# Performance work log

Measured on AMD Instinct MI355X. Metric: run time of the kernel, lower is better.

Reference implementation:

```python
import jax, jax.numpy as jnp
import numpy as np

# FTDEA(e_hidden=300, r_hidden=100, t_hidden=100)
N_NODES = 50000
N_EDGES = 250000
N_EDGES_ALL = 500000
N_REL = 300
EH, RH, TH = 300, 100, 100


def _seg_softmax(logits, seg, num):
    # torch_geometric.utils.softmax: segment-wise stable softmax
    m = jax.ops.segment_max(logits, seg, num_segments=num)
    e = jnp.exp(logits - m[seg])
    s = jax.ops.segment_sum(e, seg, num_segments=num)
    return e / s[seg]


def _gcn(x, j, i, n):
    deg = jax.ops.segment_sum(jnp.ones(i.shape[0], x.dtype), i, num_segments=n)
    dinv = jnp.where(deg > 0, 1.0 / jnp.sqrt(jnp.maximum(deg, 1.0)), 0.0)
    norm = dinv[j] * dinv[i]
    return jax.nn.relu(jax.ops.segment_sum(norm[:, None] * x[j], i, num_segments=n))


def setup_inputs():
    key = jax.random.key(0)
    ks = jax.random.split(key, 32)
    f32 = jnp.float32

    def w(k, shape):
        return jax.random.normal(k, shape, f32) / np.float32(np.sqrt(shape[0]))

    inp = {
        "x": jax.random.normal(ks[0], (N_NODES, EH), f32),
        "edge_index": jax.random.randint(ks[1], (2, N_EDGES), 0, N_NODES),
        "rel": jax.random.randint(ks[2], (N_EDGES,), 0, N_REL),
        "edge_index_all": jax.random.randint(ks[3], (2, N_EDGES_ALL), 0, N_NODES),
        "rel_size": jnp.arange(N_EDGES),
        "hw1_w": w(ks[4], (EH, EH)), "hw1_b": jnp.zeros((EH,), f32),
        "hw2_w": w(ks[5], (EH, EH)), "hw2_b": jnp.zeros((EH,), f32),
        "tc1_w": w(ks[6], (EH, TH)), "tc1_b": jnp.zeros((TH,), f32),
        "sr1_w": w(ks[7], (2 * TH, RH)), "sr1_b": jnp.zeros((RH,), f32),
        "a1_w": w(ks[8], (RH,)), "a5_w": w(ks[9], (RH,)),
        "wr_w": w(ks[10], (RH + 2 * TH, EH)), "wr_b": jnp.zeros((EH,), f32),
        "wr1_w": w(ks[11], (RH + 2 * TH, EH)), "wr1_b": jnp.zeros((EH,), f32),
        "wr2_w": w(ks[12], (RH + 2 * TH, EH)), "wr2_b": jnp.zeros((EH,), f32),
        "ah_w": w(ks[13], (EH,)), "ah1_w": w(ks[14], (EH,)), "at_w": w(ks[15], (EH,)),
        "ar1_w": w(ks[16], (EH,)), "ar2_w": w(ks[17], (EH,)), "ar3_w": w(ks[18], (EH,)),
        "ai_w": w(ks[19], (EH,)), "aj_w": w(ks[20], (EH,)),
        "fc_w": w(ks[21], (2 * EH,)), "fc_b": jnp.zeros((1,), f32),
    }
    return inp


def _forward(x, hw1_w, hw1_b, hw2_w, hw2_b, tc1_w, tc1_b, sr1_w, sr1_b, a1_w, a5_w,
             wr_w, wr_b, wr1_w, wr1_b, wr2_w, wr2_b, ah_w, ah1_w, at_w,
             ar1_w, ar2_w, ar3_w, ai_w, aj_w, fc_w, fc_b,
             edge_index, rel, edge_index_all, rel_size):
    N = x.shape[0]
    E = rel.shape[0]
    h, t = edge_index[0], edge_index[1]
    j, i = edge_index_all[0], edge_index_all[1]
    lrelu = jax.nn.leaky_relu  # slope 0.01 == F.leaky_relu default

    def highway(x1, x2, wg, bg):
        gate = jax.nn.sigmoid(x1 @ wg + bg)
        return gate * x2 + (1.0 - gate) * x1

    x = highway(x, _gcn(x, j, i, N), hw1_w, hw1_b)
    x = highway(x, _gcn(x, j, i, N), hw2_w, hw2_b)

    # --- GATt_to_R. NB: FTDEA overwrites gat_e_to_r output with zeros, so
    # x_res1 input is all-zeros and GAT_E_to_R is mathematically dead code.
    # Also r_in_t1 aliases r_in_t in the torch code, so the in-place per-relation
    # mean loop rewrites BOTH -> r_in_t1 = per-relation mean features.
    s = x @ tc1_w + tc1_b                                    # [N, t]
    cnt = jnp.maximum(jax.ops.segment_sum(jnp.ones(E, x.dtype), rel, num_segments=N_REL), 1.0)[:, None]
    mh = jax.ops.segment_sum(s[h], rel, num_segments=N_REL) / cnt
    mt = jax.ops.segment_sum(s[t], rel, num_segments=N_REL) / cnt
    r_in_t1 = jnp.concatenate([mh, mt], axis=1)[rel]         # [E, 2t]
    x_res2 = r_in_t1 @ sr1_w + sr1_b                         # [E, r]
    x_res1 = jnp.zeros((E, RH), x.dtype)                     # zeroed GAT_E_to_R output
    e1 = x_res2 @ a1_w + x_res1 @ a5_w                       # [E]
    alpha = _seg_softmax(lrelu(e1), rel, N_REL)
    x_type = jax.ops.segment_sum(alpha[:, None] * x_res2[rel_size], rel, num_segments=N_REL)  # spmm
    r_f = jnp.concatenate([x_res1 + x_type[rel], r_in_t1], axis=1)   # [E, r+2t]

    # --- GATr_to_e: three attention rounds (head, tail, head) ---
    def r2e(x_e, wr, br, a_node, a_rel, idx):
        e_r = r_f @ wr + br                                  # [E, e]
        logits = x_e[idx] @ a_node + e_r @ a_rel             # [E]
        a = _seg_softmax(lrelu(logits), idx, N)
        agg = jax.nn.relu(jax.ops.segment_sum(a[:, None] * e_r[rel_size], idx, num_segments=N))
        return x_e + agg

    x = r2e(x, wr_w, wr_b, ah_w, ar1_w, h)
    x = r2e(x, wr1_w, wr1_b, at_w, ar2_w, t)
    x = r2e(x, wr2_w, wr2_b, ah1_w, ar3_w, h)

    # --- GAT_act over edge_index_all ---
    logits = (x @ ai_w)[i] + (x @ aj_w)[j]
    a = _seg_softmax(lrelu(logits), i, N)
    g = jax.nn.relu(jax.ops.segment_sum(a[:, None] * x[j], i, num_segments=N))

    return jnp.concatenate([x, g], axis=1) @ fc_w + fc_b[0]  # [N]


def reference(x, edge_index, rel, edge_index_all, rel_size, hw1_w, hw1_b, hw2_w, hw2_b,
              tc1_w, tc1_b, sr1_w, sr1_b, a1_w, a5_w, wr_w, wr_b, wr1_w, wr1_b,
              wr2_w, wr2_b, ah_w, ah1_w, at_w, ar1_w, ar2_w, ar3_w, ai_w, aj_w, fc_w, fc_b):
    return _forward(x, hw1_w, hw1_b, hw2_w, hw2_b, tc1_w, tc1_b, sr1_w, sr1_b, a1_w, a5_w,
                    wr_w, wr_b, wr1_w, wr1_b, wr2_w, wr2_b, ah_w, ah1_w, at_w,
                    ar1_w, ar2_w, ar3_w, ai_w, aj_w, fc_w, fc_b,
                    edge_index, rel, edge_index_all, rel_size)
```

## Files before the change

### kernel.cpp

```cpp
#include <hip/hip_runtime.h>
#include <hip/hip_bf16.h>

typedef __hip_bfloat16 bf16;
typedef __attribute__((ext_vector_type(8))) short bf16x8_t;
typedef __attribute__((ext_vector_type(8))) unsigned short u16x8;
typedef __attribute__((ext_vector_type(4))) float f32x4_t;

__device__ __forceinline__ float b2f(bf16 v){ return __bfloat162float(v); }
__device__ __forceinline__ bf16 f2b(float v){ return __float2bfloat16(v); }
__device__ __forceinline__ short tobits(float v){ bf16 b = f2b(v); return *(short*)&b; }
__device__ __forceinline__ float us2f(ushort u){ return __uint_as_float(((unsigned)u)<<16); }
__device__ __forceinline__ ushort f2us(float v){ bf16 b = f2b(v); return *(ushort*)&b; }

#define NN 50000
#define NN128 50048
#define NE 250000
#define NEA 500000
#define NR 300
#define EHD 300
#define THD 100
#define RHD 100
#define XP 320
#define ERP 320
#define RCH 8
#define NBN 98
#define NBR 75
#define PREP_NB 8782
#define BCNT_NB 245

__device__ __forceinline__ int clampi(int v, int n){ return ((unsigned)v < (unsigned)n) ? v : 0; }

__device__ __forceinline__ int rdl_i(int v, int l){ return __builtin_amdgcn_readlane(v, l); }
__device__ __forceinline__ float rdl_f(float v, int l){ return __int_as_float(__builtin_amdgcn_readlane(__float_as_int(v), l)); }

typedef const __attribute__((address_space(1))) unsigned int* gas1_t;
typedef __attribute__((address_space(3))) unsigned int* las3_t;
__device__ __forceinline__ void glds16(const void* g, void* l){
    __builtin_amdgcn_global_load_lds((gas1_t)g, (las3_t)l, 16, 0, 0);
}

__device__ __forceinline__ float dpp_sum(float x){
    int v;
    v = __builtin_amdgcn_update_dpp(0, __float_as_int(x), 0x111, 0xf, 0xf, true); x += __int_as_float(v);
    v = __builtin_amdgcn_update_dpp(0, __float_as_int(x), 0x112, 0xf, 0xf, true); x += __int_as_float(v);
    v = __builtin_amdgcn_update_dpp(0, __float_as_int(x), 0x114, 0xf, 0xf, true); x += __int_as_float(v);
    v = __builtin_amdgcn_update_dpp(0, __float_as_int(x), 0x118, 0xf, 0xf, true); x += __int_as_float(v);
    v = __builtin_amdgcn_update_dpp(0, __float_as_int(x), 0x142, 0xf, 0xf, true); x += __int_as_float(v);
    v = __builtin_amdgcn_update_dpp(0, __float_as_int(x), 0x143, 0xf, 0xf, true); x += __int_as_float(v);
    return __int_as_float(__builtin_amdgcn_readlane(__float_as_int(x), 63));
}
__device__ __forceinline__ float dpp_max(float x){
    int v;
    v = __builtin_amdgcn_update_dpp(__float_as_int(x), __float_as_int(x), 0x111, 0xf, 0xf, false); x = fmaxf(x, __int_as_float(v));
    v = __builtin_amdgcn_update_dpp(__float_as_int(x), __float_as_int(x), 0x112, 0xf, 0xf, false); x = fmaxf(x, __int_as_float(v));
    v = __builtin_amdgcn_update_dpp(__float_as_int(x), __float_as_int(x), 0x114, 0xf, 0xf, false); x = fmaxf(x, __int_as_float(v));
    v = __builtin_amdgcn_update_dpp(__float_as_int(x), __float_as_int(x), 0x118, 0xf, 0xf, false); x = fmaxf(x, __int_as_float(v));
    v = __builtin_amdgcn_update_dpp(__float_as_int(x), __float_as_int(x), 0x142, 0xf, 0xf, false); x = fmaxf(x, __int_as_float(v));
    v = __builtin_amdgcn_update_dpp(__float_as_int(x), __float_as_int(x), 0x143, 0xf, 0xf, false); x = fmaxf(x, __int_as_float(v));
    return __int_as_float(__builtin_amdgcn_readlane(__float_as_int(x), 63));
}

__global__ __launch_bounds__(256) void k_prepc(const float* __restrict__ xin, ushort* __restrict__ xFu,
                       const float* __restrict__ hw1w, const float* __restrict__ hw2w,
                       const float* __restrict__ tc1w,
                       short* __restrict__ Wt1, short* __restrict__ Wt2, short* __restrict__ Wtc,
                       const float* __restrict__ ahw, const float* __restrict__ atw,
                       const float* __restrict__ ah1w, const float* __restrict__ ajw,
                       const float* __restrict__ aiw, const float* __restrict__ fcw,
                       float* __restrict__ apad, int* __restrict__ bcnt,
                       const int* __restrict__ ji, const int* __restrict__ ht,
                       const int* __restrict__ rel){
    int blk = blockIdx.x, tid = threadIdx.x;
    __shared__ int h[128];
    if(blk >= PREP_NB){
        int eb = blk - PREP_NB;
        int s = eb/BCNT_NB, bx = eb - s*BCNT_NB;
        int n_s = (s == 0) ? NEA : NE;
        int base_e = bx*2048;
        if(base_e >= n_s) return;
        int shift = (s < 3) ? 9 : 2;
        if(tid < 128) h[tid] = 0;
        __syncthreads();
        #pragma unroll
        for(int u=0;u<8;u++){
            int e = base_e + u*256 + tid;
            if(e < n_s){
                int key;
                if(s == 0) key = clampi(ji[NEA + e], NN);
                else if(s == 1) key = clampi(ht[e], NN);
                else if(s == 2) key = clampi(ht[NE + e], NN);
                else key = clampi(rel[e], NR);
                atomicAdd(&h[key >> shift], 1);
            }
        }
        __syncthreads();
        if(tid < 128 && h[tid] > 0) atomicAdd(&bcnt[s*128 + tid], h[tid]);
        return;
    }
    int i = blk*256 + tid;
    const int NC = NN*40;
    const int S1 = NC + 320*320;
    const int S2 = S1 + 320*320;
    const int S3 = S2 + 128*320;
    const int S4 = S3 + 7*XP;
    if(i < NC){
        int nrow = i/40, c8 = i - nrow*40, c = c8*8;
        ushort o[8];
        if(c + 8 <= EHD){
            const float4* src = (const float4*)(xin + (size_t)nrow*EHD + c);
            float4 v0 = src[0], v1 = src[1];
            o[0]=f2us(v0.x); o[1]=f2us(v0.y); o[2]=f2us(v0.z); o[3]=f2us(v0.w);
            o[4]=f2us(v1.x); o[5]=f2us(v1.y); o[6]=f2us(v1.z); o[7]=f2us(v1.w);
        } else {
            #pragma unroll
            for(int k=0;k<8;k++){
                int cc = c + k;
                o[k] = (cc < EHD) ? f2us(xin[(size_t)nrow*EHD + cc]) : (ushort)0;
            }
        }
        u16x8 w;
        #pragma unroll
        for(int k=0;k<8;k++) w[k] = o[k];
        *(u16x8*)(xFu + (size_t)nrow*XP + c) = w;
    } else if(i < S1){
        int ii = i - NC; int n = ii/320, k = ii - n*320;
        Wt1[ii] = (n < EHD && k < EHD) ? tobits(hw1w[(size_t)k*EHD + n]) : (short)0;
    } else if(i < S2){
        int ii = i - S1; int n = ii/320, k = ii - n*320;
        Wt2[ii] = (n < EHD && k < EHD) ? tobits(hw2w[(size_t)k*EHD + n]) : (short)0;
    } else if(i < S3){
        int ii = i - S2; int n = ii/320, k = ii - n*320;
        Wtc[ii] = (n < THD && k < EHD) ? tobits(tc1w[(size_t)k*THD + n]) : (short)0;
    } else if(i < S4){
        int ii = i - S3; int v = ii/XP, c = ii - v*XP;
        float val = 0.f;
        if(c < EHD){
            const float* src = (v==0)?ahw:(v==1)?atw:(v==2)?ah1w:(v==3)?ajw:(v==4)?aiw:
                               (v==5)? fcw : (fcw + EHD);
            val = src[c];
        }
        apad[ii] = val;
    }
}

__global__ void k_bscan(const int* __restrict__ bcnt, int* __restrict__ gbase, int* __restrict__ gcur){
    __shared__ int lds[512];
    int tid = threadIdx.x;
    int v = bcnt[tid];
    lds[tid] = v; __syncthreads();
    for(int st=1; st<128; st<<=1){
        int add = ((tid & 127) >= st) ? lds[tid-st] : 0;
        __syncthreads();
        lds[tid] += add;
        __syncthreads();
    }
    int s = tid >> 7, b = tid & 127;
    int excl = lds[tid] - v;
    gbase[s*129 + b] = excl;
    gcur[s*128 + b] = excl;
    if(b == 127) gbase[s*129 + 128] = lds[tid];
}

__global__ __launch_bounds__(256) void k_bin(const int* __restrict__ ji, const int* __restrict__ ht,
                      const int* __restrict__ rel, int* __restrict__ gcur,
                      int2* __restrict__ t0, int2* __restrict__ t1,
                      int2* __restrict__ t2, int2* __restrict__ t3){
    int s = blockIdx.y;
    int n_s = (s == 0) ? NEA : NE;
    int base_e = blockIdx.x*2048;
    if(base_e >= n_s) return;
    int shift = (s < 3) ? 9 : 2;
    int tid = threadIdx.x;
    __shared__ int cnt[128], lof[128], base[128];
    __shared__ int2 buf[2048];
    if(tid < 128) cnt[tid] = 0;
    __syncthreads();
    int kk[8], pp[8], bb[8], ss[8];
    #pragma unroll
    for(int u=0;u<8;u++){
        int e = base_e + u*256 + tid;
        bb[u] = -1;
        if(e < n_s){
            int key, pay;
            if(s == 0){ key = clampi(ji[NEA + e], NN); pay = clampi(ji[e], NN); }
            else if(s == 1){ key = clampi(ht[e], NN); pay = clampi(rel[e], NR); }
            else if(s == 2){ key = clampi(ht[NE + e], NN); pay = clampi(rel[e], NR); }
            else { key = clampi(rel[e], NR); pay = e; }
            int b = key >> shift;
            kk[u] = key; pp[u] = pay; bb[u] = b;
            ss[u] = atomicAdd(&cnt[b], 1);
        }
    }
    __syncthreads();
    if(tid == 0){
        int run = 0;
        for(int b=0;b<128;b++){ lof[b] = run; run += cnt[b]; }
    }
    __syncthreads();
    #pragma unroll
    for(int u=0;u<8;u++){
        if(bb[u] >= 0){
            int pos = lof[bb[u]] + ss[u];
            buf[pos] = make_int2(kk[u], pp[u]);
        }
    }
    __syncthreads();
    if(tid < 128 && cnt[tid] > 0) base[tid] = atomicAdd(&gcur[s*128 + tid], cnt[tid]);
    __syncthreads();
    int2* tmp = (s==0) ? t0 : (s==1) ? t1 : (s==2) ? t2 : t3;
    int total = lof[127] + cnt[127];
    for(int idx=tid; idx<total; idx+=256){
        int2 kp = buf[idx];
        int b = kp.x >> shift;
        tmp[base[b] + (idx - lof[b])] = kp;
    }
}

__global__ __launch_bounds__(256) void k_place(const int* __restrict__ gbase,
                        const int2* __restrict__ t0, const int2* __restrict__ t1,
                        const int2* __restrict__ t2, const int2* __restrict__ t3,
                        int* __restrict__ off_all, int* __restrict__ off_h,
                        int* __restrict__ off_t, int* __restrict__ off_r,
                        int* __restrict__ adj_all, int* __restrict__ adj_h,
                        int* __restrict__ adj_t, int* __restrict__ adj_r,
                        float* __restrict__ dinv){
    int s = blockIdx.y, b = blockIdx.x;
    int NB = (s < 3) ? NBN : NBR;
    if(b >= NB) return;
    int W = (s < 3) ? 512 : 4;
    int len = (s < 3) ? NN : NR;
    const int2* tmp = (s==0) ? t0 : (s==1) ? t1 : (s==2) ? t2 : t3;
    int* off = (s==0) ? off_all : (s==1) ? off_h : (s==2) ? off_t : off_r;
    int* adj = (s==0) ? adj_all : (s==1) ? adj_h : (s==2) ? adj_t : adj_r;
    int node0 = b*W;
    int node1 = node0 + W; if(node1 > len) node1 = len;
    int nloc = node1 - node0;
    int wstart = gbase[s*129 + b], wend = gbase[s*129 + b + 1];
    __shared__ int hist[512];
    __shared__ int cur[512];
    __shared__ int sb[256];
    int tid = threadIdx.x;
    for(int k=tid; k<nloc; k+=256) hist[k] = 0;
    __syncthreads();
    for(int idx = wstart + tid; idx < wend; idx += 256){
        int local = tmp[idx].x - node0;
        if((unsigned)local < (unsigned)nloc) atomicAdd(&hist[local], 1);
    }
    __syncthreads();
    int v0 = (2*tid   < nloc) ? hist[2*tid]   : 0;
    int v1 = (2*tid+1 < nloc) ? hist[2*tid+1] : 0;
    int ps = v0 + v1;
    sb[tid] = ps; __syncthreads();
    for(int st=1; st<256; st<<=1){
        int add = (tid >= st) ? sb[tid-st] : 0;
        __syncthreads();
        sb[tid] += add;
        __syncthreads();
    }
    int excl = sb[tid] - ps;
    if(2*tid < nloc){
        int o = wstart + excl;
        off[node0 + 2*tid] = o;
        cur[2*tid] = o;
        if(s == 0) dinv[node0 + 2*tid] = v0 > 0 ? rsqrtf((float)v0) : 0.f;
    }
    if(2*tid+1 < nloc){
        int o = wstart + excl + v0;
        off[node0 + 2*tid+1] = o;
        cur[2*tid+1] = o;
        if(s == 0) dinv[node0 + 2*tid+1] = v1 > 0 ? rsqrtf((float)v1) : 0.f;
    }
    if(b == NB-1 && tid == 0) off[len] = gbase[s*129 + 128];
    __syncthreads();
    for(int idx = wstart + tid; idx < wend; idx += 256){
        int2 kp = tmp[idx];
        int local = kp.x - node0;
        if((unsigned)local < (unsigned)nloc){
            int slot = atomicAdd(&cur[local], 1);
            adj[slot] = kp.y;
        }
    }
}

__global__ void k_gcn(const bf16* __restrict__ xs, bf16* __restrict__ xd,
                      const int* __restrict__ off, const int* __restrict__ adjj,
                      const float* __restrict__ dinv){
    int wid = threadIdx.x >> 6, lane = threadIdx.x & 63;
    int n = blockIdx.x*4 + wid;
    if(n >= NN) return;
    float di = dinv[n];
    int s0 = off[n], s1 = off[n+1], cnt = s1 - s0;
    bool act = lane < 40;
    float c0=0,c1=0,c2=0,c3=0,c4=0,c5=0,c6=0,c7=0;
    if(cnt > 0 && cnt <= 64){
        int jl = (lane < cnt) ? clampi(adjj[s0+lane], NN) : 0;
        float dl = (lane < cnt) ? dinv[jl] : 0.f;
        int it = 0;
        for(; it+4 <= cnt; it += 4){
            int j0=rdl_i(jl,it), j1=rdl_i(jl,it+1), j2=rdl_i(jl,it+2), j3=rdl_i(jl,it+3);
            float n0=di*rdl_f(dl,it), n1=di*rdl_f(dl,it+1), n2=di*rdl_f(dl,it+2), n3=di*rdl_f(dl,it+3);
            if(act){
                u16x8 v0 = ((const u16x8*)(xs + (size_t)j0*XP))[lane];
                u16x8 v1 = ((const u16x8*)(xs + (size_t)j1*XP))[lane];
                u16x8 v2 = ((const u16x8*)(xs + (size_t)j2*XP))[lane];
                u16x8 v3 = ((const u16x8*)(xs + (size_t)j3*XP))[lane];
                c0 += n0*us2f(v0[0])+n1*us2f(v1[0])+n2*us2f(v2[0])+n3*us2f(v3[0]);
                c1 += n0*us2f(v0[1])+n1*us2f(v1[1])+n2*us2f(v2[1])+n3*us2f(v3[1]);
                c2 += n0*us2f(v0[2])+n1*us2f(v1[2])+n2*us2f(v2[2])+n3*us2f(v3[2]);
                c3 += n0*us2f(v0[3])+n1*us2f(v1[3])+n2*us2f(v2[3])+n3*us2f(v3[3]);
                c4 += n0*us2f(v0[4])+n1*us2f(v1[4])+n2*us2f(v2[4])+n3*us2f(v3[4]);
                c5 += n0*us2f(v0[5])+n1*us2f(v1[5])+n2*us2f(v2[5])+n3*us2f(v3[5]);
                c6 += n0*us2f(v0[6])+n1*us2f(v1[6])+n2*us2f(v2[6])+n3*us2f(v3[6]);
                c7 += n0*us2f(v0[7])+n1*us2f(v1[7])+n2*us2f(v2[7])+n3*us2f(v3[7]);
            }
        }
        for(; it < cnt; it++){
            int j0 = rdl_i(jl, it);
            float n0 = di*rdl_f(dl, it);
            if(act){
                u16x8 v0 = ((const u16x8*)(xs + (size_t)j0*XP))[lane];
                c0 += n0*us2f(v0[0]); c1 += n0*us2f(v0[1]); c2 += n0*us2f(v0[2]); c3 += n0*us2f(v0[3]);
                c4 += n0*us2f(v0[4]); c5 += n0*us2f(v0[5]); c6 += n0*us2f(v0[6]); c7 += n0*us2f(v0[7]);
            }
        }
    } else if(cnt > 64){
        for(int it=s0; it<s1; it++){
            int j = clampi(adjj[it], NN);
            float nr = di * dinv[j];
            if(act){
                u16x8 v0 = ((const u16x8*)(xs + (size_t)j*XP))[lane];
                c0 += nr*us2f(v0[0]); c1 += nr*us2f(v0[1]); c2 += nr*us2f(v0[2]); c3 += nr*us2f(v0[3]);
                c4 += nr*us2f(v0[4]); c5 += nr*us2f(v0[5]); c6 += nr*us2f(v0[6]); c7 += nr*us2f(v0[7]);
            }
        }
    }
    if(act){
        u16x8 w;
        w[0]=f2us(fmaxf(c0,0.f)); w[1]=f2us(fmaxf(c1,0.f)); w[2]=f2us(fmaxf(c2,0.f)); w[3]=f2us(fmaxf(c3,0.f));
        w[4]=f2us(fmaxf(c4,0.f)); w[5]=f2us(fmaxf(c5,0.f)); w[6]=f2us(fmaxf(c6,0.f)); w[7]=f2us(fmaxf(c7,0.f));
        ((u16x8*)(xd + (size_t)n*XP))[lane] = w;
    }
}

template<int MODE>
__global__ __launch_bounds__(256) void k_gemm_mfma(const bf16* __restrict__ X,
                       const short* __restrict__ Wt, const float* __restrict__ bias,
                       bf16* __restrict__ out, const bf16* __restrict__ Xprev,
                       int M, int K, int Ncols, int ldOut, int ncb){
    __shared__ short As[64*32];
    __shared__ short Bs[64*32];
    int tid = threadIdx.x;
    int bid = blockIdx.x;
    int nwg = gridDim.x;
    int xcd = bid & 7, idx = bid >> 3;
    int q = nwg >> 3, rr = nwg & 7;
    int logical = (xcd < rr ? xcd*(q+1) : rr*(q+1) + (xcd-rr)*q) + idx;
    int pan = logical / ncb;
    int bm = pan*64, bn = (logical - pan*ncb)*64;
    int wid = tid>>6, lane = tid&63;
    int wm = (wid&1)*32, wn = (wid>>1)*32;
    int lm = lane&15, lq = lane>>4;
    f32x4_t acc00={0,0,0,0}, acc01={0,0,0,0}, acc10={0,0,0,0}, acc11={0,0,0,0};
    int srow = tid>>2, ssl = tid&3;
    int ssl_sw = ssl ^ ((srow>>1)&3);
    short* ldsA = As + (size_t)(wid*64)*8;
    short* ldsB = Bs + (size_t)(wid*64)*8;
    const bf16*  gA = X  + (size_t)(bm + srow)*K + ssl_sw*8;
    const short* gB = Wt + (size_t)(bn + srow)*K + ssl_sw*8;
    for(int k0=0; k0<K; k0+=32){
        glds16(gA + k0, ldsA);
        glds16(gB + k0, ldsB);
        __syncthreads();
        int ra0 = wm + lm, ra1 = wm + 16 + lm;
        int rb0 = wn + lm, rb1 = wn + 16 + lm;
        bf16x8_t a0 = *(const bf16x8_t*)(As + ra0*32 + ((lq ^ ((ra0>>1)&3))*8));
        bf16x8_t a1 = *(const bf16x8_t*)(As + ra1*32 + ((lq ^ ((ra1>>1)&3))*8));
        bf16x8_t b0 = *(const bf16x8_t*)(Bs + rb0*32 + ((lq ^ ((rb0>>1)&3))*8));
        bf16x8_t b1 = *(const bf16x8_t*)(Bs + rb1*32 + ((lq ^ ((rb1>>1)&3))*8));
        acc00 = __builtin_amdgcn_mfma_f32_16x16x32_bf16(a0, b0, acc00, 0, 0, 0);
        acc01 = __builtin_amdgcn_mfma_f32_16x16x32_bf16(a0, b1, acc01, 0, 0, 0);
        acc10 = __builtin_amdgcn_mfma_f32_16x16x32_bf16(a1, b0, acc10, 0, 0, 0);
        acc11 = __builtin_amdgcn_mfma_f32_16x16x32_bf16(a1, b1, acc11, 0, 0, 0);
        __syncthreads();
    }
    #pragma unroll
    for(int tm=0;tm<2;tm++){
        #pragma unroll
        for(int tn=0;tn<2;tn++){
            f32x4_t a = tm==0 ? (tn==0 ? acc00 : acc01) : (tn==0 ? acc10 : acc11);
            int gn = bn + wn + tn*16 + lm;
            if(gn >= Ncols) continue;
            float bi = bias[gn];
            #pragma unroll
            for(int r=0;r<4;r++){
                int gm = bm + wm + tm*16 + lq*4 + r;
                if(gm >= M) continue;
                float t = a[r] + bi;
                size_t p = (size_t)gm*ldOut + gn;
                if(MODE == 0){
                    out[p] = f2b(t);
                } else {
                    float g = __builtin_amdgcn_rcpf(1.f + __expf(-t));
                    out[p] = f2b(g*b2f(out[p]) + (1.f - g)*b2f(Xprev[p]));
                }
            }
        }
    }
}

__global__ void k_relsum2(const bf16* __restrict__ s, const int* __restrict__ ht,
                          const int* __restrict__ off_r, const int* __restrict__ adj_r,
                          float* __restrict__ RFpart){
    int r = blockIdx.x, c = blockIdx.y, d = threadIdx.x;
    if(d >= THD) return;
    int s0 = off_r[r], s1 = off_r[r+1];
    int cnt = s1 - s0;
    float ah = 0.f, at2 = 0.f;
    if(cnt > 0){
        int per = (cnt + RCH - 1)/RCH;
        int lo = s0 + c*per, hi = lo + per; if(hi > s1) hi = s1;
        for(int it=lo; it<hi; it++){
            int e = clampi(adj_r[it], NE);
            int hh = clampi(ht[e], NN), tt = clampi(ht[NE + e], NN);
            ah  += b2f(s[(size_t)hh*THD + d]);
            at2 += b2f(s[(size_t)tt*THD + d]);
        }
    }
    size_t base = (size_t)(r*RCH + c)*2*THD;
    RFpart[base + d] = ah;
    RFpart[base + THD + d] = at2;
}

__global__ void k_reler(const float* __restrict__ RFpart, const int* __restrict__ off_r,
                        const float* __restrict__ sr1w, const float* __restrict__ sr1b,
                        const float* w0, const float* b0, const float* w1, const float* b1,
                        const float* w2, const float* b2,
                        const float* ar1, const float* ar2, const float* ar3,
                        float* __restrict__ ER, float* __restrict__ cvec){
    int r = blockIdx.x, kk = blockIdx.y;
    const float* w = kk==0 ? w0 : (kk==1 ? w1 : w2);
    const float* b = kk==0 ? b0 : (kk==1 ? b1 : b2);
    const float* a = kk==0 ? ar1 : (kk==1 ? ar2 : ar3);
    int tid = threadIdx.x;
    __shared__ float rfs[EHD];
    int cnt = off_r[r+1] - off_r[r];
    float inv = 1.f/(float)(cnt > 1 ? cnt : 1);
    for(int d=tid; d<2*THD; d+=256){
        float sacc = 0.f;
        #pragma unroll
        for(int c=0;c<RCH;c++) sacc += RFpart[(size_t)(r*RCH + c)*2*THD + d];
        rfs[THD + d] = sacc*inv;
    }
    __syncthreads();
    if(tid < RHD){
        float v = 0.f;
        if(cnt > 0){
            v = sr1b[tid];
            for(int k2=0; k2<2*THD; k2++) v += rfs[THD + k2] * sr1w[k2*RHD + tid];
        }
        rfs[tid] = v;
    }
    __syncthreads();
    float pd = 0.f;
    for(int o = tid; o < ERP; o += 256){
        float v = 0.f;
        if(o < EHD){
            v = b[o];
            for(int d=0; d<EHD; d++) v += rfs[d] * w[(size_t)d*EHD + o];
            pd += v * a[o];
        }
        ER[((size_t)kk*NR + r)*ERP + o] = v;
    }
    __shared__ float red[4];
    pd = dpp_sum(pd);
    if((tid & 63) == 0) red[tid>>6] = pd;
    __syncthreads();
    if(tid == 0) cvec[kk*NR + r] = red[0]+red[1]+red[2]+red[3];
}

__device__ __forceinline__ void r2e_round(float* xv, bool act, int lane, int s0, int s1,
        int rl, float cval,
        const int* __restrict__ adjrel, const float* __restrict__ ERk,
        const float* __restrict__ ck, const float* __restrict__ an){
    float p = 0.f;
    if(act){
        const float4* a4 = (const float4*)an;
        float4 a0 = a4[2*lane], a1 = a4[2*lane+1];
        p = xv[0]*a0.x + xv[1]*a0.y + xv[2]*a0.z + xv[3]*a0.w
          + xv[4]*a1.x + xv[5]*a1.y + xv[6]*a1.z + xv[7]*a1.w;
    }
    p = dpp_sum(p);
    int cnt = s1 - s0;
    if(cnt <= 0) return;
    float c0=0,c1=0,c2=0,c3=0,c4=0,c5=0,c6=0,c7=0;
    if(cnt <= 64){
        float lg = p + cval;
        lg = lg > 0 ? lg : 0.01f*lg;
        float mx = dpp_max((lane < cnt) ? lg : -1e30f);
        float ex = (lane < cnt) ? __expf(lg - mx) : 0.f;
        float al = ex * __builtin_amdgcn_rcpf(dpp_sum(ex));
        int it = 0;
        for(; it+2 <= cnt; it += 2){
            int r0i = rdl_i(rl, it), r1i = rdl_i(rl, it+1);
            float q0 = rdl_f(al, it), q1 = rdl_f(al, it+1);
            if(act){
                const float4* e0p = (const float4*)(ERk + (size_t)r0i*ERP);
                const float4* e1p = (const float4*)(ERk + (size_t)r1i*ERP);
                float4 e0 = e0p[2*lane], e1 = e1p[2*lane];
                float4 f0 = e0p[2*lane+1], f1 = e1p[2*lane+1];
                c0 += q0*e0.x + q1*e1.x; c1 += q0*e0.y + q1*e1.y;
                c2 += q0*e0.z + q1*e1.z; c3 += q0*e0.w + q1*e1.w;
                c4 += q0*f0.x + q1*f1.x; c5 += q0*f0.y + q1*f1.y;
                c6 += q0*f0.z + q1*f1.z; c7 += q0*f0.w + q1*f1.w;
            }
        }
        if(it < cnt){
            int r0i = rdl_i(rl, it);
            float q0 = rdl_f(al, it);
            if(act){
                const float4* e0p = (const float4*)(ERk + (size_t)r0i*ERP);
                float4 e0 = e0p[2*lane], f0 = e0p[2*lane+1];
                c0 += q0*e0.x; c1 += q0*e0.y; c2 += q0*e0.z; c3 += q0*e0.w;
                c4 += q0*f0.x; c5 += q0*f0.y; c6 += q0*f0.z; c7 += q0*f0.w;
            }
        }
    } else {
        float mx = -1e30f;
        for(int it=s0; it<s1; it++){
            float lg = p + ck[clampi(adjrel[it], NR)];
            lg = lg > 0 ? lg : 0.01f*lg;
            mx = fmaxf(mx, lg);
        }
        float ssum = 0.f;
        for(int it=s0; it<s1; it++){
            float lg = p + ck[clampi(adjrel[it], NR)];
            lg = lg > 0 ? lg : 0.01f*lg;
            ssum += __expf(lg - mx);
        }
        float rinv = __builtin_amdgcn_rcpf(ssum);
        for(int it=s0; it<s1; it++){
            int r = clampi(adjrel[it], NR);
            float lg = p + ck[r];
            lg = lg > 0 ? lg : 0.01f*lg;
            float aw = __expf(lg - mx)*rinv;
            if(act){
                const float4* er4 = (const float4*)(ERk + (size_t)r*ERP);
                float4 e0 = er4[2*lane], f0 = er4[2*lane+1];
                c0 += aw*e0.x; c1 += aw*e0.y; c2 += aw*e0.z; c3 += aw*e0.w;
                c4 += aw*f0.x; c5 += aw*f0.y; c6 += aw*f0.z; c7 += aw*f0.w;
            }
        }
    }
    xv[0] += fmaxf(c0,0.f); xv[1] += fmaxf(c1,0.f); xv[2] += fmaxf(c2,0.f); xv[3] += fmaxf(c3,0.f);
    xv[4] += fmaxf(c4,0.f); xv[5] += fmaxf(c5,0.f); xv[6] += fmaxf(c6,0.f); xv[7] += fmaxf(c7,0.f);
}

__global__ void k_r2e3(bf16* __restrict__ x,
                       const int* __restrict__ off_h, const int* __restrict__ adj_h,
                       const int* __restrict__ off_t, const int* __restrict__ adj_t,
                       const float* __restrict__ ER, const float* __restrict__ cvec,
                       const float* __restrict__ apad, float* __restrict__ ajv){
    int wid = threadIdx.x >> 6, lane = threadIdx.x & 63;
    int n = blockIdx.x*4 + wid;
    if(n >= NN) return;
    bool act = lane < 40;
    u16x8* xr = (u16x8*)(x + (size_t)n*XP);
    float xv[8];
    if(act){
        u16x8 v = xr[lane];
        #pragma unroll
        for(int k=0;k<8;k++) xv[k] = us2f(v[k]);
    } else {
        #pragma unroll
        for(int k=0;k<8;k++) xv[k] = 0.f;
    }
    int h0 = off_h[n], h1 = off_h[n+1];
    int t0_ = off_t[n], t1_ = off_t[n+1];
    int hcnt = h1 - h0, tcnt = t1_ - t0_;
    int rlh = (hcnt > 0 && hcnt <= 64 && lane < hcnt) ? clampi(adj_h[h0+lane], NR) : 0;
    int rlt = (tcnt > 0 && tcnt <= 64 && lane < tcnt) ? clampi(adj_t[t0_+lane], NR) : 0;
    float ch1 = cvec[rlh], ctv = cvec[NR + rlt], ch3 = cvec[2*NR + rlh];
    r2e_round(xv, act, lane, h0, h1, rlh, ch1, adj_h, ER,                    cvec,      apad);
    r2e_round(xv, act, lane, t0_, t1_, rlt, ctv, adj_t, ER + (size_t)NR*ERP, cvec+NR,   apad + XP);
    r2e_round(xv, act, lane, h0, h1, rlh, ch3, adj_h, ER + (size_t)2*NR*ERP, cvec+2*NR, apad + 2*XP);
    {
        float p = 0.f;
        if(act){
            const float4* a4 = (const float4*)(apad + 3*XP);
            float4 a0 = a4[2*lane], a1 = a4[2*lane+1];
            p = xv[0]*a0.x + xv[1]*a0.y + xv[2]*a0.z + xv[3]*a0.w
              + xv[4]*a1.x + xv[5]*a1.y + xv[6]*a1.z + xv[7]*a1.w;
        }
        p = dpp_sum(p);
        if(lane == 0) ajv[n] = p;
    }
    if(act){
        u16x8 w;
        #pragma unroll
        for(int k=0;k<8;k++) w[k] = f2us(xv[k]);
        xr[lane] = w;
    }
}

__global__ void k_final(const bf16* __restrict__ x, const float* __restrict__ ajv,
                        const int* __restrict__ off, const int* __restrict__ adjj,
                        const float* __restrict__ apad, const float* __restrict__ fcb,
                        float* __restrict__ out){
    int wid = threadIdx.x >> 6, lane = threadIdx.x & 63;
    int n = blockIdx.x*4 + wid;
    if(n >= NN) return;
    bool act = lane < 40;
    float xv[8];
    if(act){
        u16x8 v = ((const u16x8*)(x + (size_t)n*XP))[lane];
        #pragma unroll
        for(int k=0;k<8;k++) xv[k] = us2f(v[k]);
    } else {
        #pragma unroll
        for(int k=0;k<8;k++) xv[k] = 0.f;
    }
    float p = 0.f;
    if(act){
        const float4* a4 = (const float4*)(apad + 4*XP);
        float4 a0 = a4[2*lane], a1 = a4[2*lane+1];
        p = xv[0]*a0.x + xv[1]*a0.y + xv[2]*a0.z + xv[3]*a0.w
          + xv[4]*a1.x + xv[5]*a1.y + xv[6]*a1.z + xv[7]*a1.w;
    }
    p = dpp_sum(p);
    int s0 = off[n], s1 = off[n+1], cnt = s1 - s0;
    float c0=0,c1=0,c2=0,c3=0,c4=0,c5=0,c6=0,c7=0;
    if(cnt > 0 && cnt <= 64){
        int jl = (lane < cnt) ? clampi(adjj[s0+lane], NN) : 0;
        float av = (lane < cnt) ? ajv[jl] : 0.f;
        float lg = p + av;
        lg = lg > 0 ? lg : 0.01f*lg;
        float mx = dpp_max((lane < cnt) ? lg : -1e30f);
        float ex = (lane < cnt) ? __expf(lg - mx) : 0.f;
        float al = ex * __builtin_amdgcn_rcpf(dpp_sum(ex));
        int it = 0;
        for(; it+4 <= cnt; it += 4){
            int j0=rdl_i(jl,it), j1=rdl_i(jl,it+1), j2=rdl_i(jl,it+2), j3=rdl_i(jl,it+3);
            float q0=rdl_f(al,it), q1=rdl_f(al,it+1), q2=rdl_f(al,it+2), q3=rdl_f(al,it+3);
            if(act){
                u16x8 v0 = ((const u16x8*)(x + (size_t)j0*XP))[lane];
                u16x8 v1 = ((const u16x8*)(x + (size_t)j1*XP))[lane];
                u16x8 v2 = ((const u16x8*)(x + (size_t)j2*XP))[lane];
                u16x8 v3 = ((const u16x8*)(x + (size_t)j3*XP))[lane];
                c0 += q0*us2f(v0[0])+q1*us2f(v1[0])+q2*us2f(v2[0])+q3*us2f(v3[0]);
                c1 += q0*us2f(v0[1])+q1*us2f(v1[1])+q2*us2f(v2[1])+q3*us2f(v3[1]);
                c2 += q0*us2f(v0[2])+q1*us2f(v1[2])+q2*us2f(v2[2])+q3*us2f(v3[2]);
                c3 += q0*us2f(v0[3])+q1*us2f(v1[3])+q2*us2f(v2[3])+q3*us2f(v3[3]);
                c4 += q0*us2f(v0[4])+q1*us2f(v1[4])+q2*us2f(v2[4])+q3*us2f(v3[4]);
                c5 += q0*us2f(v0[5])+q1*us2f(v1[5])+q2*us2f(v2[5])+q3*us2f(v3[5]);
                c6 += q0*us2f(v0[6])+q1*us2f(v1[6])+q2*us2f(v2[6])+q3*us2f(v3[6]);
                c7 += q0*us2f(v0[7])+q1*us2f(v1[7])+q2*us2f(v2[7])+q3*us2f(v3[7]);
            }
        }
        for(; it < cnt; it++){
            int j0 = rdl_i(jl, it);
            float q0 = rdl_f(al, it);
            if(act){
                u16x8 v0 = ((const u16x8*)(x + (size_t)j0*XP))[lane];
                c0 += q0*us2f(v0[0]); c1 += q0*us2f(v0[1]); c2 += q0*us2f(v0[2]); c3 += q0*us2f(v0[3]);
                c4 += q0*us2f(v0[4]); c5 += q0*us2f(v0[5]); c6 += q0*us2f(v0[6]); c7 += q0*us2f(v0[7]);
            }
        }
    } else if(cnt > 64){
        float mx = -1e30f;
        for(int it=s0; it<s1; it++){
            float lg = p + ajv[clampi(adjj[it], NN)];
            lg = lg > 0 ? lg : 0.01f*lg;
            mx = fmaxf(mx, lg);
        }
        float ssum = 0.f;
        for(int it=s0; it<s1; it++){
            float lg = p + ajv[clampi(adjj[it], NN)];
            lg = lg > 0 ? lg : 0.01f*lg;
            ssum += __expf(lg - mx);
        }
        float rinv = __builtin_amdgcn_rcpf(ssum);
        for(int it=s0; it<s1; it++){
            int j = clampi(adjj[it], NN);
            float lg = p + ajv[j];
            lg = lg > 0 ? lg : 0.01f*lg;
            float aw = __expf(lg - mx)*rinv;
            if(act){
                u16x8 v0 = ((const u16x8*)(x + (size_t)j*XP))[lane];
                c0 += aw*us2f(v0[0]); c1 += aw*us2f(v0[1]); c2 += aw*us2f(v0[2]); c3 += aw*us2f(v0[3]);
                c4 += aw*us2f(v0[4]); c5 += aw*us2f(v0[5]); c6 += aw*us2f(v0[6]); c7 += aw*us2f(v0[7]);
            }
        }
    }
    float part = 0.f;
    if(act){
        const float4* f5 = (const float4*)(apad + 5*XP);
        const float4* f6 = (const float4*)(apad + 6*XP);
        float4 u0 = f5[2*lane], u1 = f5[2*lane+1];
        float4 g0 = f6[2*lane], g1 = f6[2*lane+1];
        part = xv[0]*u0.x + xv[1]*u0.y + xv[2]*u0.z + xv[3]*u0.w
             + xv[4]*u1.x + xv[5]*u1.y + xv[6]*u1.z + xv[7]*u1.w
             + fmaxf(c0,0.f)*g0.x + fmaxf(c1,0.f)*g0.y + fmaxf(c2,0.f)*g0.z + fmaxf(c3,0.f)*g0.w
             + fmaxf(c4,0.f)*g1.x + fmaxf(c5,0.f)*g1.y + fmaxf(c6,0.f)*g1.z + fmaxf(c7,0.f)*g1.w;
    }
    part = dpp_sum(part);
    if(lane == 0) out[n] = part + fcb[0];
}

extern "C" void kernel_launch(void* const* d_in, const int* in_sizes, int n_in,
                              void* d_out, int out_size, void* d_ws, size_t ws_size,
                              hipStream_t stream){
    const float* x_in = (const float*)d_in[0];
    const int*  ht   = (const int*)d_in[1];
    const int*  rel  = (const int*)d_in[2];
    const int*  ji   = (const int*)d_in[3];
    const float* hw1w=(const float*)d_in[5];  const float* hw1b=(const float*)d_in[6];
    const float* hw2w=(const float*)d_in[7];  const float* hw2b=(const float*)d_in[8];
    const float* tc1w=(const float*)d_in[9];  const float* tc1b=(const float*)d_in[10];
    const float* sr1w=(const float*)d_in[11]; const float* sr1b=(const float*)d_in[12];
    const float* wrw =(const float*)d_in[15]; const float* wrb =(const float*)d_in[16];
    const float* wr1w=(const float*)d_in[17]; const float* wr1b=(const float*)d_in[18];
    const float* wr2w=(const float*)d_in[19]; const float* wr2b=(const float*)d_in[20];
    const float* ahw =(const float*)d_in[21]; const float* ah1w=(const float*)d_in[22];
    const float* atw =(const float*)d_in[23];
    const float* ar1 =(const float*)d_in[24]; const float* ar2 =(const float*)d_in[25];
    const float* ar3 =(const float*)d_in[26];
    const float* aiw =(const float*)d_in[27]; const float* ajw =(const float*)d_in[28];
    const float* fcw =(const float*)d_in[29]; const float* fcb =(const float*)d_in[30];
    float* out = (float*)d_out;

    char* w = (char*)d_ws;
    auto alloc = [&](size_t bytes)->char*{ char* p = w; w += (bytes + 255)/256*256; return p; };
    bf16* xF = (bf16*)alloc((size_t)NN128*XP*2);
    bf16* B  = (bf16*)alloc((size_t)NN128*XP*2);
    char* Bc = (char*)B;
    int2* tmp_all = (int2*)(Bc);
    int2* tmp_h   = (int2*)(Bc + 4u*1024*1024);
    int2* tmp_t   = (int2*)(Bc + 8u*1024*1024);
    int2* tmp_r   = (int2*)(Bc + 12u*1024*1024);
    bf16*  sbuf   = (bf16*)(Bc);
    float* RFpart = (float*)(Bc + 12u*1024*1024);
    float* ER     = (float*)(Bc + 14u*1024*1024);
    float* cvec   = (float*)(Bc + 15u*1024*1024 + 512u*1024);
    float* ajv    = (float*)(Bc + 16u*1024*1024);
    short* Wt1 = (short*)alloc((size_t)320*320*2);
    short* Wt2 = (short*)alloc((size_t)320*320*2);
    short* Wtc = (short*)alloc((size_t)128*320*2);
    float* apad = (float*)alloc((size_t)7*XP*4);
    float* dinv = (float*)alloc((size_t)NN*4);
    int* off_all=(int*)alloc((NN+1)*4);
    int* adj_all=(int*)alloc((size_t)NEA*4);
    int* off_h  =(int*)alloc((NN+1)*4);
    int* adj_h  =(int*)alloc((size_t)NE*4);
    int* off_t  =(int*)alloc((NN+1)*4);
    int* adj_t  =(int*)alloc((size_t)NE*4);
    int* off_r  =(int*)alloc((NR+1)*4);
    int* adj_r  =(int*)alloc((size_t)NE*4);
    int* bcnt   =(int*)alloc(512*4);
    int* gbase  =(int*)alloc(4*129*4);
    int* gcur   =(int*)alloc(4*128*4);

    hipMemsetAsync(bcnt, 0, 512*4, stream);
    k_prepc<<<dim3(PREP_NB + 4*BCNT_NB), dim3(256), 0, stream>>>(x_in, (ushort*)xF, hw1w, hw2w, tc1w,
                                                          Wt1, Wt2, Wtc,
                                                          ahw, atw, ah1w, ajw, aiw, fcw,
                                                          apad, bcnt, ji, ht, rel);
    k_bscan<<<dim3(1), dim3(512), 0, stream>>>(bcnt, gbase, gcur);
    k_bin<<<dim3((NEA+2047)/2048, 4), dim3(256), 0, stream>>>(ji, ht, rel, gcur,
                                                              tmp_all, tmp_h, tmp_t, tmp_r);
    k_place<<<dim3(NBN, 4), dim3(256), 0, stream>>>(gbase, tmp_all, tmp_h, tmp_t, tmp_r,
                                                    off_all, off_h, off_t, off_r,
                                                    adj_all, adj_h, adj_t, adj_r, dinv);

    const int nb4 = (NN+3)/4;
    k_gcn<<<dim3(nb4), dim3(256), 0, stream>>>(xF, B, off_all, adj_all, dinv);
    k_gemm_mfma<1><<<dim3((NN128/64)*5), dim3(256), 0, stream>>>(xF, Wt1, hw1b, B, xF, NN, XP, EHD, XP, 5);
    k_gcn<<<dim3(nb4), dim3(256), 0, stream>>>(B, xF, off_all, adj_all, dinv);
    k_gemm_mfma<1><<<dim3((NN128/64)*5), dim3(256), 0, stream>>>(B, Wt2, hw2b, xF, B, NN, XP, EHD, XP, 5);
    k_gemm_mfma<0><<<dim3((NN128/64)*2), dim3(256), 0, stream>>>(xF, Wtc, tc1b, sbuf, xF, NN, XP, THD, THD, 2);
    k_relsum2<<<dim3(NR, RCH), dim3(128), 0, stream>>>(sbuf, ht, off_r, adj_r, RFpart);
    k_reler<<<dim3(NR, 3), dim3(256), 0, stream>>>(RFpart, off_r, sr1w, sr1b,
                                                   wrw, wrb, wr1w, wr1b, wr2w, wr2b,
                                                   ar1, ar2, ar3, ER, cvec);
    k_r2e3<<<dim3(nb4), dim3(256), 0, stream>>>(xF, off_h, adj_h, off_t, adj_t, ER, cvec,
                                                apad, ajv);
    k_final<<<dim3(nb4), dim3(256), 0, stream>>>(xF, ajv, off_all, adj_all, apad, fcb, out);
}
```

Baseline: 610.7 us.

## Run GCN aggregation and highway gate GEMM in one launch, combine separately

Merges the GCN neighbor aggregation and the highway gate GEMM into a single kernel. Block IDs pick which branch a block runs, so the two independent stages run at the same time instead of back to back. The sigmoid gate is written to a new buffer G, and a small elementwise kernel then blends the gate with the aggregated and previous features. This lets the memory-bound gather overlap with the MFMA GEMM. The cost is an extra full-size gate buffer write and read plus one more launch per layer.

```diff
diff --git a/kernel.cpp b/kernel.cpp
--- a/kernel.cpp
+++ b/kernel.cpp
@@ -27,6 +27,8 @@
 #define NBR 75
 #define PREP_NB 8782
 #define BCNT_NB 245
+#define NB4 12500
+#define GBHW 3910
 
 __device__ __forceinline__ int clampi(int v, int n){ return ((unsigned)v < (unsigned)n) ? v : 0; }
 
@@ -282,70 +284,144 @@
     }
 }
 
-__global__ void k_gcn(const bf16* __restrict__ xs, bf16* __restrict__ xd,
-                      const int* __restrict__ off, const int* __restrict__ adjj,
-                      const float* __restrict__ dinv){
-    int wid = threadIdx.x >> 6, lane = threadIdx.x & 63;
-    int n = blockIdx.x*4 + wid;
-    if(n >= NN) return;
-    float di = dinv[n];
-    int s0 = off[n], s1 = off[n+1], cnt = s1 - s0;
-    bool act = lane < 40;
-    float c0=0,c1=0,c2=0,c3=0,c4=0,c5=0,c6=0,c7=0;
-    if(cnt > 0 && cnt <= 64){
-        int jl = (lane < cnt) ? clampi(adjj[s0+lane], NN) : 0;
-        float dl = (lane < cnt) ? dinv[jl] : 0.f;
-        int it = 0;
-        for(; it+4 <= cnt; it += 4){
-            int j0=rdl_i(jl,it), j1=rdl_i(jl,it+1), j2=rdl_i(jl,it+2), j3=rdl_i(jl,it+3);
-            float n0=di*rdl_f(dl,it), n1=di*rdl_f(dl,it+1), n2=di*rdl_f(dl,it+2), n3=di*rdl_f(dl,it+3);
-            if(act){
-                u16x8 v0 = ((const u16x8*)(xs + (size_t)j0*XP))[lane];
-                u16x8 v1 = ((const u16x8*)(xs + (size_t)j1*XP))[lane];
-                u16x8 v2 = ((const u16x8*)(xs + (size_t)j2*XP))[lane];
-                u16x8 v3 = ((const u16x8*)(xs + (size_t)j3*XP))[lane];
-                c0 += n0*us2f(v0[0])+n1*us2f(v1[0])+n2*us2f(v2[0])+n3*us2f(v3[0]);
-                c1 += n0*us2f(v0[1])+n1*us2f(v1[1])+n2*us2f(v2[1])+n3*us2f(v3[1]);
-                c2 += n0*us2f(v0[2])+n1*us2f(v1[2])+n2*us2f(v2[2])+n3*us2f(v3[2]);
-                c3 += n0*us2f(v0[3])+n1*us2f(v1[3])+n2*us2f(v2[3])+n3*us2f(v3[3]);
-                c4 += n0*us2f(v0[4])+n1*us2f(v1[4])+n2*us2f(v2[4])+n3*us2f(v3[4]);
-                c5 += n0*us2f(v0[5])+n1*us2f(v1[5])+n2*us2f(v2[5])+n3*us2f(v3[5]);
-                c6 += n0*us2f(v0[6])+n1*us2f(v1[6])+n2*us2f(v2[6])+n3*us2f(v3[6]);
-                c7 += n0*us2f(v0[7])+n1*us2f(v1[7])+n2*us2f(v2[7])+n3*us2f(v3[7]);
-            }
-        }
-        for(; it < cnt; it++){
-            int j0 = rdl_i(jl, it);
-            float n0 = di*rdl_f(dl, it);
-            if(act){
-                u16x8 v0 = ((const u16x8*)(xs + (size_t)j0*XP))[lane];
-                c0 += n0*us2f(v0[0]); c1 += n0*us2f(v0[1]); c2 += n0*us2f(v0[2]); c3 += n0*us2f(v0[3]);
-                c4 += n0*us2f(v0[4]); c5 += n0*us2f(v0[5]); c6 += n0*us2f(v0[6]); c7 += n0*us2f(v0[7]);
-            }
-        }
-    } else if(cnt > 64){
-        for(int it=s0; it<s1; it++){
-            int j = clampi(adjj[it], NN);
-            float nr = di * dinv[j];
-            if(act){
-                u16x8 v0 = ((const u16x8*)(xs + (size_t)j*XP))[lane];
-                c0 += nr*us2f(v0[0]); c1 += nr*us2f(v0[1]); c2 += nr*us2f(v0[2]); c3 += nr*us2f(v0[3]);
-                c4 += nr*us2f(v0[4]); c5 += nr*us2f(v0[5]); c6 += nr*us2f(v0[6]); c7 += nr*us2f(v0[7]);
-            }
-        }
-    }
-    if(act){
-        u16x8 w;
-        w[0]=f2us(fmaxf(c0,0.f)); w[1]=f2us(fmaxf(c1,0.f)); w[2]=f2us(fmaxf(c2,0.f)); w[3]=f2us(fmaxf(c3,0.f));
-        w[4]=f2us(fmaxf(c4,0.f)); w[5]=f2us(fmaxf(c5,0.f)); w[6]=f2us(fmaxf(c6,0.f)); w[7]=f2us(fmaxf(c7,0.f));
-        ((u16x8*)(xd + (size_t)n*XP))[lane] = w;
-    }
-}
-
-template<int MODE>
+__global__ __launch_bounds__(256) void k_hw(const bf16* __restrict__ xs, bf16* __restrict__ xd,
+                       bf16* __restrict__ gate, const short* __restrict__ Wt,
+                       const float* __restrict__ bias,
+                       const int* __restrict__ off, const int* __restrict__ adjj,
+                       const float* __restrict__ dinv){
+    __shared__ short As[64*32];
+    __shared__ short Bs[64*32];
+    int bid = blockIdx.x;
+    int tid = threadIdx.x;
+    if(bid < NB4){
+        int wid = tid >> 6, lane = tid & 63;
+        int n = bid*4 + wid;
+        if(n >= NN) return;
+        float di = dinv[n];
+        int s0 = off[n], s1 = off[n+1], cnt = s1 - s0;
+        bool act = lane < 40;
+        float c0=0,c1=0,c2=0,c3=0,c4=0,c5=0,c6=0,c7=0;
+        if(cnt > 0 && cnt <= 64){
+            int jl = (lane < cnt) ? clampi(adjj[s0+lane], NN) : 0;
+            float dl = (lane < cnt) ? dinv[jl] : 0.f;
+            int it = 0;
+            for(; it+4 <= cnt; it += 4){
+                int j0=rdl_i(jl,it), j1=rdl_i(jl,it+1), j2=rdl_i(jl,it+2), j3=rdl_i(jl,it+3);
+                float n0=di*rdl_f(dl,it), n1=di*rdl_f(dl,it+1), n2=di*rdl_f(dl,it+2), n3=di*rdl_f(dl,it+3);
+                if(act){
+                    u16x8 v0 = ((const u16x8*)(xs + (size_t)j0*XP))[lane];
+                    u16x8 v1 = ((const u16x8*)(xs + (size_t)j1*XP))[lane];
+                    u16x8 v2 = ((const u16x8*)(xs + (size_t)j2*XP))[lane];
+                    u16x8 v3 = ((const u16x8*)(xs + (size_t)j3*XP))[lane];
+                    c0 += n0*us2f(v0[0])+n1*us2f(v1[0])+n2*us2f(v2[0])+n3*us2f(v3[0]);
+                    c1 += n0*us2f(v0[1])+n1*us2f(v1[1])+n2*us2f(v2[1])+n3*us2f(v3[1]);
+                    c2 += n0*us2f(v0[2])+n1*us2f(v1[2])+n2*us2f(v2[2])+n3*us2f(v3[2]);
+                    c3 += n0*us2f(v0[3])+n1*us2f(v1[3])+n2*us2f(v2[3])+n3*us2f(v3[3]);
+                    c4 += n0*us2f(v0[4])+n1*us2f(v1[4])+n2*us2f(v2[4])+n3*us2f(v3[4]);
+                    c5 += n0*us2f(v0[5])+n1*us2f(v1[5])+n2*us2f(v2[5])+n3*us2f(v3[5]);
+                    c6 += n0*us2f(v0[6])+n1*us2f(v1[6])+n2*us2f(v2[6])+n3*us2f(v3[6]);
+                    c7 += n0*us2f(v0[7])+n1*us2f(v1[7])+n2*us2f(v2[7])+n3*us2f(v3[7]);
+                }
+            }
+            for(; it < cnt; it++){
+                int j0 = rdl_i(jl, it);
+                float n0 = di*rdl_f(dl, it);
+                if(act){
+                    u16x8 v0 = ((const u16x8*)(xs + (size_t)j0*XP))[lane];
+                    c0 += n0*us2f(v0[0]); c1 += n0*us2f(v0[1]); c2 += n0*us2f(v0[2]); c3 += n0*us2f(v0[3]);
+                    c4 += n0*us2f(v0[4]); c5 += n0*us2f(v0[5]); c6 += n0*us2f(v0[6]); c7 += n0*us2f(v0[7]);
+                }
+            }
+        } else if(cnt > 64){
+            for(int it=s0; it<s1; it++){
+                int j = clampi(adjj[it], NN);
+                float nr = di * dinv[j];
+                if(act){
+                    u16x8 v0 = ((const u16x8*)(xs + (size_t)j*XP))[lane];
+                    c0 += nr*us2f(v0[0]); c1 += nr*us2f(v0[1]); c2 += nr*us2f(v0[2]); c3 += nr*us2f(v0[3]);
+                    c4 += nr*us2f(v0[4]); c5 += nr*us2f(v0[5]); c6 += nr*us2f(v0[6]); c7 += nr*us2f(v0[7]);
+                }
+            }
+        }
+        if(act){
+            u16x8 w;
+            w[0]=f2us(fmaxf(c0,0.f)); w[1]=f2us(fmaxf(c1,0.f)); w[2]=f2us(fmaxf(c2,0.f)); w[3]=f2us(fmaxf(c3,0.f));
+            w[4]=f2us(fmaxf(c4,0.f)); w[5]=f2us(fmaxf(c5,0.f)); w[6]=f2us(fmaxf(c6,0.f)); w[7]=f2us(fmaxf(c7,0.f));
+            ((u16x8*)(xd + (size_t)n*XP))[lane] = w;
+        }
+        return;
+    }
+    int g = bid - NB4;
+    int xcd = g & 7, idx = g >> 3;
+    const int q = GBHW >> 3, r = GBHW & 7;
+    int logical = (xcd < r ? xcd*(q+1) : r*(q+1) + (xcd-r)*q) + idx;
+    int pan = logical/5;
+    int bm = pan*64, bn = (logical - pan*5)*64;
+    int wid = tid>>6, lane = tid&63;
+    int wm = (wid&1)*32, wn = (wid>>1)*32;
+    int lm = lane&15, lq = lane>>4;
+    f32x4_t acc00={0,0,0,0}, acc01={0,0,0,0}, acc10={0,0,0,0}, acc11={0,0,0,0};
+    int srow = tid>>2, ssl = tid&3;
+    int ssl_sw = ssl ^ ((srow>>1)&3);
+    short* ldsA = As + (size_t)(wid*64)*8;
+    short* ldsB = Bs + (size_t)(wid*64)*8;
+    const bf16*  gA = xs + (size_t)(bm + srow)*XP + ssl_sw*8;
+    const short* gB = Wt + (size_t)(bn + srow)*XP + ssl_sw*8;
+    for(int k0=0; k0<XP; k0+=32){
+        glds16(gA + k0, ldsA);
+        glds16(gB + k0, ldsB);
+        __syncthreads();
+        int ra0 = wm + lm, ra1 = wm + 16 + lm;
+        int rb0 = wn + lm, rb1 = wn + 16 + lm;
+        bf16x8_t a0 = *(const bf16x8_t*)(As + ra0*32 + ((lq ^ ((ra0>>1)&3))*8));
+        bf16x8_t a1 = *(const bf16x8_t*)(As + ra1*32 + ((lq ^ ((ra1>>1)&3))*8));
+        bf16x8_t b0 = *(const bf16x8_t*)(Bs + rb0*32 + ((lq ^ ((rb0>>1)&3))*8));
+        bf16x8_t b1 = *(const bf16x8_t*)(Bs + rb1*32 + ((lq ^ ((rb1>>1)&3))*8));
+        acc00 = __builtin_amdgcn_mfma_f32_16x16x32_bf16(a0, b0, acc00, 0, 0, 0);
+        acc01 = __builtin_amdgcn_mfma_f32_16x16x32_bf16(a0, b1, acc01, 0, 0, 0);
+        acc10 = __builtin_amdgcn_mfma_f32_16x16x32_bf16(a1, b0, acc10, 0, 0, 0);
+        acc11 = __builtin_amdgcn_mfma_f32_16x16x32_bf16(a1, b1, acc11, 0, 0, 0);
+        __syncthreads();
+    }
+    #pragma unroll
+    for(int tm=0;tm<2;tm++){
+        #pragma unroll
+        for(int tn=0;tn<2;tn++){
+            f32x4_t a = tm==0 ? (tn==0 ? acc00 : acc01) : (tn==0 ? acc10 : acc11);
+            int gn = bn + wn + tn*16 + lm;
+            float bi = (gn < EHD) ? bias[gn] : 0.f;
+            #pragma unroll
+            for(int rr2=0;rr2<4;rr2++){
+                int gm = bm + wm + tm*16 + lq*4 + rr2;
+                if(gm >= NN) continue;
+                float t = a[rr2] + bi;
+                float gv = (gn < EHD) ? __builtin_amdgcn_rcpf(1.f + __expf(-t)) : 0.f;
+                gate[(size_t)gm*XP + gn] = f2b(gv);
+            }
+        }
+    }
+}
+
+__global__ __launch_bounds__(256) void k_comb(const bf16* __restrict__ g, const bf16* __restrict__ bnew,
+                       const bf16* __restrict__ xprev, bf16* __restrict__ dst){
+    int idx = blockIdx.x*256 + threadIdx.x;
+    if(idx >= NN*40) return;
+    size_t o = (size_t)idx*8;
+    u16x8 gv = *(const u16x8*)((const ushort*)g + o);
+    u16x8 bv = *(const u16x8*)((const ushort*)bnew + o);
+    u16x8 xv = *(const u16x8*)((const ushort*)xprev + o);
+    u16x8 w;
+    #pragma unroll
+    for(int k=0;k<8;k++){
+        float gg = us2f(gv[k]);
+        w[k] = f2us(gg*us2f(bv[k]) + (1.f-gg)*us2f(xv[k]));
+    }
+    *(u16x8*)((ushort*)dst + o) = w;
+}
+
 __global__ __launch_bounds__(256) void k_gemm_mfma(const bf16* __restrict__ X,
                        const short* __restrict__ Wt, const float* __restrict__ bias,
-                       bf16* __restrict__ out, const bf16* __restrict__ Xprev,
+                       bf16* __restrict__ out,
                        int M, int K, int Ncols, int ldOut, int ncb){
     __shared__ short As[64*32];
     __shared__ short Bs[64*32];
@@ -392,17 +468,10 @@
             if(gn >= Ncols) continue;
             float bi = bias[gn];
             #pragma unroll
-            for(int r=0;r<4;r++){
-                int gm = bm + wm + tm*16 + lq*4 + r;
+            for(int r2=0;r2<4;r2++){
+                int gm = bm + wm + tm*16 + lq*4 + r2;
                 if(gm >= M) continue;
-                float t = a[r] + bi;
-                size_t p = (size_t)gm*ldOut + gn;
-                if(MODE == 0){
-                    out[p] = f2b(t);
-                } else {
-                    float g = __builtin_amdgcn_rcpf(1.f + __expf(-t));
-                    out[p] = f2b(g*b2f(out[p]) + (1.f - g)*b2f(Xprev[p]));
-                }
+                out[(size_t)gm*ldOut + gn] = f2b(a[r2] + bi);
             }
         }
     }
@@ -732,6 +801,7 @@
     auto alloc = [&](size_t bytes)->char*{ char* p = w; w += (bytes + 255)/256*256; return p; };
     bf16* xF = (bf16*)alloc((size_t)NN128*XP*2);
     bf16* B  = (bf16*)alloc((size_t)NN128*XP*2);
+    bf16* G  = (bf16*)alloc((size_t)NN128*XP*2);
     char* Bc = (char*)B;
     int2* tmp_all = (int2*)(Bc);
     int2* tmp_h   = (int2*)(Bc + 4u*1024*1024);
@@ -771,17 +841,17 @@
                                                     off_all, off_h, off_t, off_r,
                                                     adj_all, adj_h, adj_t, adj_r, dinv);
 
-    const int nb4 = (NN+3)/4;
-    k_gcn<<<dim3(nb4), dim3(256), 0, stream>>>(xF, B, off_all, adj_all, dinv);
-    k_gemm_mfma<1><<<dim3((NN128/64)*5), dim3(256), 0, stream>>>(xF, Wt1, hw1b, B, xF, NN, XP, EHD, XP, 5);
-    k_gcn<<<dim3(nb4), dim3(256), 0, stream>>>(B, xF, off_all, adj_all, dinv);
-    k_gemm_mfma<1><<<dim3((NN128/64)*5), dim3(256), 0, stream>>>(B, Wt2, hw2b, xF, B, NN, XP, EHD, XP, 5);
-    k_gemm_mfma<0><<<dim3((NN128/64)*2), dim3(256), 0, stream>>>(xF, Wtc, tc1b, sbuf, xF, NN, XP, THD, THD, 2);
+    const int CB = (NN*40 + 255)/256;
+    k_hw<<<dim3(NB4 + GBHW), dim3(256), 0, stream>>>(xF, B, G, Wt1, hw1b, off_all, adj_all, dinv);
+    k_comb<<<dim3(CB), dim3(256), 0, stream>>>(G, B, xF, B);
+    k_hw<<<dim3(NB4 + GBHW), dim3(256), 0, stream>>>(B, xF, G, Wt2, hw2b, off_all, adj_all, dinv);
+    k_comb<<<dim3(CB), dim3(256), 0, stream>>>(G, xF, B, xF);
+    k_gemm_mfma<<<dim3((NN128/64)*2), dim3(256), 0, stream>>>(xF, Wtc, tc1b, sbuf, NN, XP, THD, THD, 2);
     k_relsum2<<<dim3(NR, RCH), dim3(128), 0, stream>>>(sbuf, ht, off_r, adj_r, RFpart);
     k_reler<<<dim3(NR, 3), dim3(256), 0, stream>>>(RFpart, off_r, sr1w, sr1b,
                                                    wrw, wrb, wr1w, wr1b, wr2w, wr2b,
                                                    ar1, ar2, ar3, ER, cvec);
-    k_r2e3<<<dim3(nb4), dim3(256), 0, stream>>>(xF, off_h, adj_h, off_t, adj_t, ER, cvec,
+    k_r2e3<<<dim3(NB4), dim3(256), 0, stream>>>(xF, off_h, adj_h, off_t, adj_t, ER, cvec,
                                                 apad, ajv);
-    k_final<<<dim3(nb4), dim3(256), 0, stream>>>(xF, ajv, off_all, adj_all, apad, fcb, out);
-}
+    k_final<<<dim3(NB4), dim3(256), 0, stream>>>(xF, ajv, off_all, adj_all, apad, fcb, out);
+}
```

New measurement: 633.7 us. +3.8%, slower.
